# Kernel tuning notes

Measured on AMD Instinct MI355X. Metric: run time of the kernel, lower is better.

## Reference

```python
import jax, jax.numpy as jnp
import numpy as np

GROUPS = 4
BN_EPS = 1e-5


def conv2d(x, w, pad=0):
    return jax.lax.conv_general_dilated(x, w, (1, 1), [(pad, pad), (pad, pad)],
                                        dimension_numbers=('NCHW', 'OIHW', 'NCHW'))


def bn_infer(x, g, b, m, v):
    s = g * jax.lax.rsqrt(v + BN_EPS)
    return x * s[None, :, None, None] + (b - m * s)[None, :, None, None]


def refine_residual(x, w1, w3a, g, b, m, v, w3b):
    # RefineResidual(has_relu=True): 1x1 -> ConvBnRelu(3x3) -> 3x3 conv, residual, relu
    x1 = conv2d(x, w1)
    t = jax.nn.relu(bn_infer(conv2d(x1, w3a, pad=1), g, b, m, v))
    t = conv2d(t, w3b, pad=1)
    return jax.nn.relu(t + x1)


def grid_edges(H, W):
    # 4-connected pixel grid: right + down neighbors
    idx = np.arange(H * W).reshape(H, W)
    eu = np.concatenate([idx[:, :-1].ravel(), idx[:-1, :].ravel()]).astype(np.int32)
    ev = np.concatenate([idx[:, 1:].ravel(), idx[1:, :].ravel()]).astype(np.int32)
    return jnp.asarray(eu), jnp.asarray(ev)


def boruvka_mst(w, eu, ev, N):
    # Boruvka MST over the grid graph; returns bool mask over edges (N-1 True).
    E = w.shape[0]
    nodes = jnp.arange(N, dtype=jnp.int32)
    order = jnp.argsort(w).astype(jnp.int32)                  # edge ids by weight (unique ranks)
    rank = jnp.zeros(E, jnp.int32).at[order].set(jnp.arange(E, dtype=jnp.int32))
    BIG = jnp.int32(E)
    R = int(np.ceil(np.log2(max(N, 2)))) + 2

    def flatten(p):
        return jax.lax.fori_loop(0, R, lambda _, q: q[q], p)

    def body(_, state):
        parent, mst = state
        cu, cv = parent[eu], parent[ev]
        key = jnp.where(cu != cv, rank, BIG)
        cmin = jnp.minimum(jax.ops.segment_min(key, cu, num_segments=N),
                           jax.ops.segment_min(key, cv, num_segments=N))
        valid = cmin < BIG
        e = order[jnp.minimum(cmin, E - 1)]                   # min outgoing edge per component
        mst = mst.at[e].max(valid)
        other = jnp.where(cu[e] == nodes, cv[e], cu[e])
        pnew = jnp.where(valid, other, nodes)
        # break mutual (2-cycle) merges: smaller label becomes root
        pnew = jnp.where((pnew[pnew] == nodes) & (nodes < pnew), nodes, pnew)
        return flatten(pnew), mst

    _, mst = jax.lax.fori_loop(0, R + 2, body, (nodes, jnp.zeros(E, bool)))
    return mst


def root_and_depth(mst, eu, ev, N):
    # BFS-root the tree at node 0 -> parent pointers, then depth by pointer doubling.
    pn = jnp.full(N, -1, jnp.int32).at[0].set(0)

    def bfs(_, pn):
        vis = pn >= 0
        a = mst & vis[eu] & (~vis[ev])
        b = mst & vis[ev] & (~vis[eu])
        pn = pn.at[ev].max(jnp.where(a, eu, jnp.int32(-1)))
        pn = pn.at[eu].max(jnp.where(b, ev, jnp.int32(-1)))
        return pn

    pn = jax.lax.fori_loop(0, N, bfs, pn)
    R = int(np.ceil(np.log2(max(N, 2)))) + 2
    d0 = (jnp.arange(N) != 0).astype(jnp.int32)

    def dbl(_, s):
        d, p = s
        return d + d[p], p[p]

    depth, _ = jax.lax.fori_loop(0, R, dbl, (d0, pn))
    return pn, depth


def tree_filter_group(x, w, pn, depth):
    # Exact O(N) two-pass tree filter: y_i = sum_j prod(path weights i->j) x_j.
    # x: [N, C] (ones channel appended by caller), w: [N] edge weight to parent.
    N = x.shape[0]
    notroot = jnp.arange(N) != 0

    def up(i, agg):                                           # leaves -> root
        lev = N - 1 - i
        sel = (depth == lev) & notroot
        return agg.at[pn].add(jnp.where(sel[:, None], w[:, None] * agg, 0.0))

    agg = jax.lax.fori_loop(0, N - 1, up, x)

    def down(lev, F):                                         # root -> leaves
        cand = agg + w[:, None] * (F[pn] - w[:, None] * agg)
        return jnp.where(((depth == lev) & notroot)[:, None], cand, F)

    return jax.lax.fori_loop(1, N, down, agg)


def tree_filter_2d(feat, emb, pn, depth):
    # Grouped normalized tree filtering (TreeFilter2D): per-group edge affinity
    # exp(-||e_v - e_parent(v)||^2); normalize by filtering an all-ones channel.
    B, C, H, W = feat.shape
    N = H * W
    f = feat.reshape(B, GROUPS, C // GROUPS, N)
    e = emb.reshape(B, GROUPS, -1, N)

    def per_batch(fb, eb, pnb, db):
        w = jnp.exp(-jnp.sum((eb - eb[:, :, pnb]) ** 2, axis=1))   # [G, N]
        x = jnp.concatenate([fb, jnp.ones_like(fb[:, :1])], axis=1)
        x = jnp.swapaxes(x, 1, 2)                                  # [G, N, Cg+1]
        out = jax.vmap(lambda xg, wg: tree_filter_group(xg, wg, pnb, db))(x, w)
        y = out[..., :-1] / out[..., -1:]
        return jnp.swapaxes(y, 1, 2)

    out = jax.vmap(per_batch)(f, e, pn, depth)
    return out.reshape(B, C, H, W)


def _forward(fm, last_fm, lat_w1, lat_w3a, lat_g, lat_b, lat_m, lat_v, lat_w3b,
             ref_w1, ref_w3a, ref_g, ref_b, ref_m, ref_v, ref_w3b, emb_w):
    B, Cb, H, W = fm.shape
    N = H * W
    eu, ev = grid_edges(H, W)
    latent = refine_residual(fm, lat_w1, lat_w3a, lat_g, lat_b, lat_m, lat_v, lat_w3b)
    # MinimumSpanningTree(norm2_distance) on backbone features fm
    f = fm.reshape(B, Cb, N)
    dist = jnp.sum((f[:, :, eu] - f[:, :, ev]) ** 2, axis=1)       # [B, E]
    mst = jax.vmap(lambda d: boruvka_mst(d, eu, ev, N))(dist)
    pn, depth = jax.vmap(lambda m: root_and_depth(m, eu, ev, N))(mst)
    embed = conv2d(last_fm, emb_w)                                 # embed_layer (1x1, no bn/relu)
    fusion = latent + tree_filter_2d(last_fm, embed, pn, depth)
    return refine_residual(fusion, ref_w1, ref_w3a, ref_g, ref_b, ref_m, ref_v, ref_w3b)


def setup_inputs() -> dict:
    key = jax.random.key(0)
    ks = jax.random.split(key, 12)
    B, Cb, Cbiz, Cemb, H, W = 2, 1024, 64, 32, 32, 32
    r = lambda k, s: jax.random.normal(k, s, jnp.float32) * 0.05
    return dict(
        fm=jax.random.normal(ks[0], (B, Cb, H, W), jnp.float32),
        last_fm=jax.random.normal(ks[1], (B, Cbiz, H, W), jnp.float32),
        lat_w1=r(ks[2], (Cbiz, Cb, 1, 1)),
        lat_w3a=r(ks[3], (Cbiz, Cbiz, 3, 3)),
        lat_g=jnp.ones(Cbiz, jnp.float32),
        lat_b=jnp.zeros(Cbiz, jnp.float32),
        lat_m=jnp.zeros(Cbiz, jnp.float32),
        lat_v=jax.random.uniform(ks[4], (Cbiz,), jnp.float32, 0.5, 1.5),
        lat_w3b=r(ks[5], (Cbiz, Cbiz, 3, 3)),
        ref_w1=r(ks[6], (Cbiz, Cbiz, 1, 1)),
        ref_w3a=r(ks[7], (Cbiz, Cbiz, 3, 3)),
        ref_g=jnp.ones(Cbiz, jnp.float32),
        ref_b=jnp.zeros(Cbiz, jnp.float32),
        ref_m=jnp.zeros(Cbiz, jnp.float32),
        ref_v=jax.random.uniform(ks[8], (Cbiz,), jnp.float32, 0.5, 1.5),
        ref_w3b=r(ks[9], (Cbiz, Cbiz, 3, 3)),
        emb_w=r(ks[10], (Cemb, Cbiz, 1, 1)),
    )


def reference(fm, last_fm, lat_w1, lat_w3a, lat_g, lat_b, lat_m, lat_v, lat_w3b,
              ref_w1, ref_w3a, ref_g, ref_b, ref_m, ref_v, ref_w3b, emb_w):
    return _forward(fm, last_fm, lat_w1, lat_w3a, lat_g, lat_b, lat_m, lat_v, lat_w3b,
                    ref_w1, ref_w3a, ref_g, ref_b, ref_m, ref_v, ref_w3b, emb_w)
```

## Files before the change

### kernel.cpp

```cpp
#include <hip/hip_runtime.h>
#include <hip/hip_bf16.h>

#define NN 1024
#define EE 1984

__device__ __forceinline__ void edge_uv(int e, int* u, int* v) {
    if (e < 992) {
        int r = e / 31, c = e - r * 31;
        *u = r * 32 + c; *v = *u + 1;
    } else {
        *u = e - 992; *v = *u + 32;
    }
}

__device__ void conv1x1_tile(const float* __restrict__ in, const float* __restrict__ in2,
                             const float* __restrict__ w,
                             float* __restrict__ out, int CIN, int Cout,
                             int b, int co0, int n0, float* red) {
    int tid = threadIdx.x;
    int px = tid & 63, kc = tid >> 6;
    int kcu = __builtin_amdgcn_readfirstlane(kc);
    int KCH = CIN >> 4;
    size_t ibase = (size_t)b * CIN * NN + n0 + px;
    const float* wr = w + (size_t)co0 * CIN;
    float acc[8] = {0.f,0.f,0.f,0.f,0.f,0.f,0.f,0.f};
    for (int ci = kcu * KCH; ci < kcu * KCH + KCH; ++ci) {
        float xv = in[ibase + (size_t)ci * NN];
        if (in2) xv += in2[ibase + (size_t)ci * NN];
#pragma unroll
        for (int j = 0; j < 8; ++j)
            acc[j] += wr[j * CIN + ci] * xv;
    }
#pragma unroll
    for (int j = 0; j < 8; ++j) red[j * 1024 + tid] = acc[j];
    __syncthreads();
    for (int s = 8; s >= 1; s >>= 1) {
        if (kc < s) {
#pragma unroll
            for (int j = 0; j < 8; ++j)
                red[j * 1024 + kc * 64 + px] += red[j * 1024 + (kc + s) * 64 + px];
        }
        __syncthreads();
    }
    if (kc == 0) {
        size_t ob = ((size_t)b * Cout + co0) * NN + n0 + px;
#pragma unroll
        for (int j = 0; j < 8; ++j) out[ob + (size_t)j * NN] = red[j * 1024 + px];
    }
}

__device__ void dist_tile(const float* __restrict__ fm, float* __restrict__ dist,
                          int b, int eb, float* red) {
    int tid = threadIdx.x;
    int le = tid & 63, kc = tid >> 6;
    int kcu = __builtin_amdgcn_readfirstlane(kc);
    int e = eb * 64 + le;
    int u, v; edge_uv(e, &u, &v);
    const float* fp = fm + (size_t)b * 1024 * NN;
    float s = 0.f;
    for (int c = kcu * 64; c < kcu * 64 + 64; ++c) {
        float d = fp[(size_t)c * NN + u] - fp[(size_t)c * NN + v];
        s += d * d;
    }
    red[tid] = s;
    __syncthreads();
    for (int ss = 8; ss >= 1; ss >>= 1) {
        if (kc < ss) red[kc * 64 + le] += red[(kc + ss) * 64 + le];
        __syncthreads();
    }
    if (kc == 0) dist[b * EE + e] = red[le];
}

__device__ void conv3x3_body(const float* __restrict__ in, const float* __restrict__ w,
                             const float* __restrict__ gg, const float* __restrict__ bb,
                             const float* __restrict__ mm, const float* __restrict__ vv,
                             const float* __restrict__ res, float* __restrict__ out,
                             int mode, int b, int co, int r0, float* pl) {
    int tid = threadIdx.x;
    const float* ip = in + (size_t)b * 64 * NN;
    const float* wp = w + (size_t)co * 64 * 9;
    int r = tid >> 5, c = tid & 31;
    float acc = 0.f;
    for (int h = 0; h < 2; ++h) {
        __syncthreads();
        for (int i4 = tid; i4 < 32 * 80; i4 += 256) {
            int ci = i4 / 80, o = i4 - ci * 80;
            int row = r0 - 1 + (o >> 3), c4 = (o & 7) << 2;
            float4 val = make_float4(0.f, 0.f, 0.f, 0.f);
            if (row >= 0 && row < 32)
                val = *(const float4*)&ip[(size_t)(h * 32 + ci) * NN + row * 32 + c4];
            *(float4*)&pl[ci * 320 + (o >> 3) * 32 + c4] = val;
        }
        __syncthreads();
        for (int ci = 0; ci < 32; ++ci) {
            float wv[9];
#pragma unroll
            for (int q = 0; q < 9; ++q) wv[q] = wp[(h * 32 + ci) * 9 + q];
            float s = 0.f;
#pragma unroll
            for (int dy = 0; dy < 3; ++dy) {
                const float* row = &pl[ci * 320 + (r + dy) * 32];
#pragma unroll
                for (int dx = -1; dx <= 1; ++dx) {
                    int cc = c + dx;
                    float xv = (cc >= 0 && cc < 32) ? row[cc] : 0.f;
                    s += wv[dy * 3 + (dx + 1)] * xv;
                }
            }
            acc += s;
        }
    }
    float val;
    size_t op = ((size_t)b * 64 + co) * NN + r0 * 32 + tid;
    if (mode == 0) {
        float sc = gg[co] * rsqrtf(vv[co] + 1e-5f);
        val = acc * sc + (bb[co] - mm[co] * sc);
    } else {
        val = acc + res[op];
    }
    out[op] = fmaxf(val, 0.f);
}

struct MstS {
    unsigned long long minkey[NN];
    unsigned long long ekey[EE];
    int parent[NN], pnw[NN], pn[NN], dep[NN], scr[NN], elist[NN];
    int mstm[EE];
    int cnt, cnt2;
};

__device__ void mst_body_1024(const float* __restrict__ dist, int b, MstS* S,
                              int* __restrict__ pn_g, int* __restrict__ maxd_g,
                              int* __restrict__ ord_g, int* __restrict__ off_g) {
    int tid = threadIdx.x;
    const float* wb = dist + b * EE;
    S->parent[tid] = tid;
    S->minkey[tid] = ~0ULL;
    for (int e = tid; e < EE; e += 1024) {
        S->mstm[e] = 0;
        S->ekey[e] = ((unsigned long long)__float_as_uint(wb[e]) << 32) | (unsigned)e;
    }
    if (tid == 0) { S->cnt = 0; S->cnt2 = 0; }
    __syncthreads();

    int r = tid >> 5, c = tid & 31;
    int* P = S->parent;
    int* Q = S->pnw;
    for (int round = 0; round < 14; ++round) {
        int pv = P[tid];
        unsigned long long mk = ~0ULL;
        if (c < 31 && P[tid + 1] != pv) {
            unsigned long long k = S->ekey[r * 31 + c]; if (k < mk) mk = k;
        }
        if (c > 0 && P[tid - 1] != pv) {
            unsigned long long k = S->ekey[r * 31 + c - 1]; if (k < mk) mk = k;
        }
        if (r < 31 && P[tid + 32] != pv) {
            unsigned long long k = S->ekey[992 + r * 32 + c]; if (k < mk) mk = k;
        }
        if (r > 0 && P[tid - 32] != pv) {
            unsigned long long k = S->ekey[992 + (r - 1) * 32 + c]; if (k < mk) mk = k;
        }
        if (mk != ~0ULL) atomicMin(&S->minkey[pv], mk);
        __syncthreads();

        unsigned long long sel = S->minkey[tid];
        int np;
        if (sel != ~0ULL) {
            int e = (int)(sel & 0xffffffffULL);
            if (atomicExch(&S->mstm[e], 1) == 0) atomicAdd(&S->cnt, 1);
            int eu, ev; edge_uv(e, &eu, &ev);
            int cu = P[eu], cv = P[ev];
            np = (cu == tid) ? cv : cu;
        } else np = tid;
        int q = np, pq;
        if (q == tid) pq = tid;
        else {
            unsigned long long selq = S->minkey[q];
            if (selq != ~0ULL) {
                int e2 = (int)(selq & 0xffffffffULL);
                int eu2, ev2; edge_uv(e2, &eu2, &ev2);
                int cu2 = P[eu2], cv2 = P[ev2];
                pq = (cu2 == q) ? cv2 : cu2;
            } else pq = q;
        }
        Q[tid] = (pq == tid && tid < q) ? tid : q;
        __syncthreads();

        bool first = true;
        for (;;) {
            if (first) { S->minkey[tid] = ~0ULL; first = false; }
            int p = Q[tid];
            p = Q[p]; p = Q[p]; p = Q[p];
            Q[tid] = p;
            int ch = (Q[p] != p);
            if (!__syncthreads_or(ch)) break;
        }
        if (S->cnt == NN - 1) break;
        int* t = P; P = Q; Q = t;
    }

    for (int e = tid; e < EE; e += 1024)
        if (S->mstm[e]) { int s = atomicAdd(&S->cnt2, 1); S->elist[s] = e; }
    __syncthreads();
    int ecnt = S->cnt2;

    S->pn[tid] = (tid == 0) ? 0 : -1;
    __syncthreads();
    volatile int* vpn = S->pn;
    int myu = 0, myv = 0; bool have = tid < ecnt;
    if (have) { edge_uv(S->elist[tid], &myu, &myv); }
    for (;;) {
        int ch = 0;
        for (int s = 0; s < 24; ++s) {
            if (have) {
                int pu = vpn[myu], pv = vpn[myv];
                if (pu >= 0 && pv < 0)      { vpn[myv] = myu; ch = 1; }
                else if (pv >= 0 && pu < 0) { vpn[myu] = myv; ch = 1; }
            }
        }
        if (!__syncthreads_or(ch)) break;
    }
    int incomplete = __syncthreads_or(S->pn[tid] < 0);

    S->dep[tid] = (tid != 0) ? 1 : 0;
    S->pnw[tid] = S->pn[tid];
    __syncthreads();
    int* dA = S->dep;  int* dB = (int*)S->ekey;
    int* pA = S->pnw;  int* pB = ((int*)S->ekey) + NN;
    for (int it = 0; it < 12; ++it) {
        int p = pA[tid];
        int j = (p < 0) ? (NN + p) : p;
        dB[tid] = dA[tid] + dA[j];
        int nx = pA[j];
        pB[tid] = nx;
        int anynz = __syncthreads_or(nx != 0);
        int* t = dA; dA = dB; dB = t;
        t = pA; pA = pB; pB = t;
        if (!incomplete && !anynz) break;
    }
    if (tid == 0) S->cnt = 0;
    __syncthreads();
    int d = dA[tid];
    if (d >= 1 && d <= NN - 1) atomicMax(&S->cnt, d);
    __syncthreads();
    int maxd = S->cnt;

    S->scr[tid] = 0;
    __syncthreads();
    int bkt = (tid != 0 && d >= 1 && d <= NN - 1) ? d : 0;
    atomicAdd(&S->scr[bkt], 1);
    __syncthreads();
    int cntv = S->scr[tid];
    int lane = tid & 63, wid = tid >> 6;
    int x = cntv;
    for (int d2 = 1; d2 < 64; d2 <<= 1) {
        int y = __shfl_up(x, d2, 64);
        if (lane >= d2) x += y;
    }
    if (lane == 63) S->pnw[wid] = x;
    __syncthreads();
    if (tid < 16) {
        int off = 0;
        for (int i = 0; i < tid; ++i) off += S->pnw[i];
        S->parent[tid] = off;
    }
    __syncthreads();
    int excl = x - cntv + S->parent[wid];
    int* mi = (int*)S->minkey;
    mi[tid] = excl;
    S->scr[tid] = excl;
    __syncthreads();
    int pos = atomicAdd(&S->scr[bkt], 1);
    S->elist[pos] = tid;
    __syncthreads();

    pn_g[b * NN + tid]    = S->pn[tid];
    ord_g[b * NN + tid]   = S->elist[tid];
    off_g[b * 1025 + tid] = mi[tid];
    if (tid == 0) { off_g[b * 1025 + 1024] = NN; maxd_g[b] = maxd; }
}

struct TfSmem { float agg[NN * 3]; float wv[NN]; int jj[NN]; int ords[NN]; int offs[1025]; };
__device__ void treefilter_wave(const float* __restrict__ feat, const float* __restrict__ emb,
                                const int* __restrict__ pn_g, const int* __restrict__ ord_g,
                                const int* __restrict__ off_g, const int* __restrict__ maxd_g,
                                float* __restrict__ tfout, int b, int g, int sub, TfSmem* S) {
    int lane = threadIdx.x;
    const float* eb = emb + ((size_t)b * 32 + g * 8) * NN;
    int c0 = g * 16 + sub * 2;
    const float* fb = feat + ((size_t)b * 64 + c0) * NN;
    for (int k = 0; k < 16; ++k) {
        int v = lane + k * 64;
        int p = pn_g[b * NN + v];
        int j = (p < 0) ? (NN + p) : p;
        S->jj[v] = j;
        float s = 0.f;
#pragma unroll
        for (int q = 0; q < 8; ++q) {
            float d = eb[(size_t)q * NN + v] - eb[(size_t)q * NN + j];
            s += d * d;
        }
        S->wv[v] = expf(-s);
        S->agg[v * 3 + 0] = fb[v];
        S->agg[v * 3 + 1] = fb[NN + v];
        S->agg[v * 3 + 2] = 1.f;
        S->ords[v] = ord_g[b * NN + v];
        S->offs[v] = off_g[b * 1025 + v];
    }
    if (lane == 0) S->offs[1024] = NN;
    int maxdep = maxd_g[b];
    for (int lev = maxdep; lev >= 1; --lev) {
        int s0 = S->offs[lev], s1 = S->offs[lev + 1];
        for (int i = s0 + lane; i < s1; i += 64) {
            int v = S->ords[i]; int j = S->jj[v]; float w = S->wv[v];
            atomicAdd(&S->agg[j * 3 + 0], w * S->agg[v * 3 + 0]);
            atomicAdd(&S->agg[j * 3 + 1], w * S->agg[v * 3 + 1]);
            atomicAdd(&S->agg[j * 3 + 2], w * S->agg[v * 3 + 2]);
        }
    }
    for (int lev = 1; lev <= maxdep; ++lev) {
        int s0 = S->offs[lev], s1 = S->offs[lev + 1];
        for (int i = s0 + lane; i < s1; i += 64) {
            int v = S->ords[i]; int j = S->jj[v]; float w = S->wv[v];
#pragma unroll
            for (int c = 0; c < 3; ++c) {
                float a = S->agg[v * 3 + c];
                S->agg[v * 3 + c] = a + w * (S->agg[j * 3 + c] - w * a);
            }
        }
    }
    float* ob = tfout + ((size_t)b * 64 + c0) * NN;
    for (int k = 0; k < 16; ++k) {
        int v = lane + k * 64;
        float inv = 1.f / S->agg[v * 3 + 2];
        ob[v]      = S->agg[v * 3 + 0] * inv;
        ob[NN + v] = S->agg[v * 3 + 1] * inv;
    }
}

__global__ __launch_bounds__(1024) void k0_dist(
    const float* __restrict__ fm, float* __restrict__ dist) {
    __shared__ float red[1024];
    int i = blockIdx.x;
    dist_tile(fm, dist, i / 31, i % 31, red);
}

union K1S { float red[8192]; MstS m; };
__global__ __launch_bounds__(1024) void k1_fused(
    const float* __restrict__ fm, const float* __restrict__ last_fm,
    const float* __restrict__ lat_w1, const float* __restrict__ emb_w,
    float* __restrict__ lat_x1, float* __restrict__ embed,
    const float* __restrict__ dist, int* __restrict__ pn_g,
    int* __restrict__ maxd_g, int* __restrict__ ord_g, int* __restrict__ off_g) {
    __shared__ __align__(16) K1S s;
    int bx = blockIdx.x;
    if (bx < 2) {
        mst_body_1024(dist, bx, &s.m, pn_g, maxd_g, ord_g, off_g);
    } else if (bx < 258) {
        int i = bx - 2, b = i >> 7, r = i & 127;
        conv1x1_tile(fm, nullptr, lat_w1, lat_x1, 1024, 64,
                     b, (r >> 4) * 8, (r & 15) * 64, s.red);
    } else {
        int i = bx - 258, b = i >> 6, r = i & 63;
        conv1x1_tile(last_fm, nullptr, emb_w, embed, 64, 32,
                     b, (r >> 4) * 8, (r & 15) * 64, s.red);
    }
}

union K2S { float pl[32 * 320]; TfSmem t; };
__global__ __launch_bounds__(256) void k2_fused(
    const float* __restrict__ lat_x1, const float* __restrict__ lat_w3a,
    const float* __restrict__ lat_g, const float* __restrict__ lat_b,
    const float* __restrict__ lat_m, const float* __restrict__ lat_v,
    float* __restrict__ lat_t1,
    const float* __restrict__ last_fm, const float* __restrict__ embed,
    const int* __restrict__ pn_g, const int* __restrict__ ord_g,
    const int* __restrict__ off_g, const int* __restrict__ maxd_g,
    float* __restrict__ tfout) {
    __shared__ __align__(16) K2S s;
    int bx = blockIdx.x;
    if (bx < 64) {
        if (threadIdx.x >= 64) return;
        treefilter_wave(last_fm, embed, pn_g, ord_g, off_g, maxd_g, tfout,
                        bx >> 5, (bx >> 3) & 3, bx & 7, &s.t);
    } else {
        int i = bx - 64, b = i >> 8, co = (i >> 2) & 63, r0 = (i & 3) * 8;
        conv3x3_body(lat_x1, lat_w3a, lat_g, lat_b, lat_m, lat_v,
                     nullptr, lat_t1, 0, b, co, r0, s.pl);
    }
}

__global__ __launch_bounds__(256) void conv3x3_kernel(
    const float* __restrict__ in, const float* __restrict__ w,
    const float* __restrict__ gg, const float* __restrict__ bb,
    const float* __restrict__ mm, const float* __restrict__ vv,
    const float* __restrict__ res, float* __restrict__ out, int mode) {
    __shared__ __align__(16) float pl[32 * 320];
    conv3x3_body(in, w, gg, bb, mm, vv, res, out, mode,
                 blockIdx.z, blockIdx.y, blockIdx.x * 8, pl);
}

__global__ __launch_bounds__(1024) void conv1x1_add_kernel(
    const float* __restrict__ in, const float* __restrict__ in2,
    const float* __restrict__ w, float* __restrict__ out, int CIN, int Cout) {
    __shared__ float red[8192];
    conv1x1_tile(in, in2, w, out, CIN, Cout, blockIdx.z, blockIdx.y * 8,
                 blockIdx.x * 64, red);
}

extern "C" void kernel_launch(void* const* d_in, const int* in_sizes, int n_in,
                              void* d_out, int out_size, void* d_ws, size_t ws_size,
                              hipStream_t stream) {
    const float* fm      = (const float*)d_in[0];
    const float* last_fm = (const float*)d_in[1];
    const float* lat_w1  = (const float*)d_in[2];
    const float* lat_w3a = (const float*)d_in[3];
    const float* lat_g   = (const float*)d_in[4];
    const float* lat_b   = (const float*)d_in[5];
    const float* lat_m   = (const float*)d_in[6];
    const float* lat_v   = (const float*)d_in[7];
    const float* lat_w3b = (const float*)d_in[8];
    const float* ref_w1  = (const float*)d_in[9];
    const float* ref_w3a = (const float*)d_in[10];
    const float* ref_g   = (const float*)d_in[11];
    const float* ref_b   = (const float*)d_in[12];
    const float* ref_m   = (const float*)d_in[13];
    const float* ref_v   = (const float*)d_in[14];
    const float* ref_w3b = (const float*)d_in[15];
    const float* emb_w   = (const float*)d_in[16];
    float* out = (float*)d_out;

    float* ws      = (float*)d_ws;
    float* lat_x1  = ws;
    float* lat_t1  = lat_x1 + 131072;
    float* latent  = lat_t1 + 131072;
    float* dist    = latent + 131072;
    float* embed   = dist + 4096;
    float* tfout   = embed + 65536;
    float* ref_x1  = tfout + 131072;
    float* ref_t1  = ref_x1 + 131072;
    int*   pn      = (int*)(ref_t1 + 131072);
    int*   ordg    = pn + 2048;
    int*   offg    = ordg + 2048;
    int*   maxd    = offg + 2080;

    k0_dist<<<62, 1024, 0, stream>>>(fm, dist);
    k1_fused<<<386, 1024, 0, stream>>>(fm, last_fm, lat_w1, emb_w,
                                       lat_x1, embed, dist, pn, maxd, ordg, offg);
    k2_fused<<<576, 256, 0, stream>>>(lat_x1, lat_w3a, lat_g, lat_b, lat_m, lat_v,
                                      lat_t1, last_fm, embed, pn, ordg, offg,
                                      maxd, tfout);
    conv3x3_kernel<<<dim3(4, 64, 2), 256, 0, stream>>>(
        lat_t1, lat_w3b, nullptr, nullptr, nullptr, nullptr, lat_x1, latent, 1);
    conv1x1_add_kernel<<<dim3(16, 8, 2), 1024, 0, stream>>>(
        latent, tfout, ref_w1, ref_x1, 64, 64);
    conv3x3_kernel<<<dim3(4, 64, 2), 256, 0, stream>>>(
        ref_x1, ref_w3a, ref_g, ref_b, ref_m, ref_v, nullptr, ref_t1, 0);
    conv3x3_kernel<<<dim3(4, 64, 2), 256, 0, stream>>>(
        ref_t1, ref_w3b, nullptr, nullptr, nullptr, nullptr, ref_x1, out, 1);
}
```

Before: 244.3 us.

## Fold refine 1x1 into 3x3 weights and regroup stages into five launches

Precomputes a contracted weight (ref_w3a composed with ref_w1) so the refine 3x3 conv reads latent+tfout directly instead of waiting on the 1x1 output. That 3x3 conv then runs alongside the 1x1 in one launch. The stages are regrouped so that dist and lat 1x1 share the first kernel, the MST overlaps the lat 3x3a conv (now full-image 1024-thread blocks), and the lat 3x3b conv overlaps the tree filter. The goal is fewer launches and more overlap of the serial MST and tree-filter work with convs. The cost is extra FLOPs for the contraction and added 3x3 work on 64 input channels.

Measured after the change: 226.5 us. 7.3% less time.

```diff
diff --git a/kernel.cpp b/kernel.cpp
--- a/kernel.cpp
+++ b/kernel.cpp
@@ -13,7 +13,7 @@
     }
 }
 
-__device__ void conv1x1_tile(const float* __restrict__ in, const float* __restrict__ in2,
+__device__ void conv1x1_tile(const float* __restrict__ in,
                              const float* __restrict__ w,
                              float* __restrict__ out, int CIN, int Cout,
                              int b, int co0, int n0, float* red) {
@@ -26,7 +26,6 @@
     float acc[8] = {0.f,0.f,0.f,0.f,0.f,0.f,0.f,0.f};
     for (int ci = kcu * KCH; ci < kcu * KCH + KCH; ++ci) {
         float xv = in[ibase + (size_t)ci * NN];
-        if (in2) xv += in2[ibase + (size_t)ci * NN];
 #pragma unroll
         for (int j = 0; j < 8; ++j)
             acc[j] += wr[j * CIN + ci] * xv;
@@ -47,6 +46,24 @@
 #pragma unroll
         for (int j = 0; j < 8; ++j) out[ob + (size_t)j * NN] = red[j * 1024 + px];
     }
+}
+
+__device__ void conv1x1_64(const float* __restrict__ in, const float* __restrict__ in2,
+                           const float* __restrict__ w, float* __restrict__ out,
+                           int b, int co0, int px0) {
+    int tid = threadIdx.x;
+    size_t ibase = (size_t)b * 64 * NN + px0 + tid;
+    const float* wr = w + (size_t)co0 * 64;
+    float acc[8] = {0.f,0.f,0.f,0.f,0.f,0.f,0.f,0.f};
+    for (int ci = 0; ci < 64; ++ci) {
+        float xv = in[ibase + (size_t)ci * NN] + in2[ibase + (size_t)ci * NN];
+#pragma unroll
+        for (int j = 0; j < 8; ++j)
+            acc[j] += wr[j * 64 + ci] * xv;
+    }
+    size_t ob = ((size_t)b * 64 + co0) * NN + px0 + tid;
+#pragma unroll
+    for (int j = 0; j < 8; ++j) out[ob + (size_t)j * NN] = acc[j];
 }
 
 __device__ void dist_tile(const float* __restrict__ fm, float* __restrict__ dist,
@@ -71,13 +88,26 @@
     if (kc == 0) dist[b * EE + e] = red[le];
 }
 
-__device__ void conv3x3_body(const float* __restrict__ in, const float* __restrict__ w,
+__device__ void wc_contract(const float* __restrict__ w3a, const float* __restrict__ w1,
+                            float* __restrict__ wc, int co) {
+    int t = threadIdx.x;
+    if (t >= 576) return;
+    int ci = t / 9, q = t - ci * 9;
+    float s = 0.f;
+    for (int cm = 0; cm < 64; ++cm)
+        s += w3a[((size_t)co * 64 + cm) * 9 + q] * w1[cm * 64 + ci];
+    wc[((size_t)co * 64 + ci) * 9 + q] = s;
+}
+
+__device__ void conv3x3_body(const float* __restrict__ in, const float* __restrict__ in2,
+                             const float* __restrict__ w,
                              const float* __restrict__ gg, const float* __restrict__ bb,
                              const float* __restrict__ mm, const float* __restrict__ vv,
                              const float* __restrict__ res, float* __restrict__ out,
                              int mode, int b, int co, int r0, float* pl) {
     int tid = threadIdx.x;
     const float* ip = in + (size_t)b * 64 * NN;
+    const float* ip2 = in2 ? in2 + (size_t)b * 64 * NN : nullptr;
     const float* wp = w + (size_t)co * 64 * 9;
     int r = tid >> 5, c = tid & 31;
     float acc = 0.f;
@@ -87,8 +117,14 @@
             int ci = i4 / 80, o = i4 - ci * 80;
             int row = r0 - 1 + (o >> 3), c4 = (o & 7) << 2;
             float4 val = make_float4(0.f, 0.f, 0.f, 0.f);
-            if (row >= 0 && row < 32)
-                val = *(const float4*)&ip[(size_t)(h * 32 + ci) * NN + row * 32 + c4];
+            if (row >= 0 && row < 32) {
+                size_t off = (size_t)(h * 32 + ci) * NN + row * 32 + c4;
+                val = *(const float4*)&ip[off];
+                if (ip2) {
+                    float4 v2 = *(const float4*)&ip2[off];
+                    val.x += v2.x; val.y += v2.y; val.z += v2.z; val.w += v2.w;
+                }
+            }
             *(float4*)&pl[ci * 320 + (o >> 3) * 32 + c4] = val;
         }
         __syncthreads();
@@ -112,6 +148,55 @@
     }
     float val;
     size_t op = ((size_t)b * 64 + co) * NN + r0 * 32 + tid;
+    if (mode == 0) {
+        float sc = gg[co] * rsqrtf(vv[co] + 1e-5f);
+        val = acc * sc + (bb[co] - mm[co] * sc);
+    } else {
+        val = acc + res[op];
+    }
+    out[op] = fmaxf(val, 0.f);
+}
+
+__device__ void conv3x3_1024(const float* __restrict__ in, const float* __restrict__ w,
+                             const float* __restrict__ gg, const float* __restrict__ bb,
+                             const float* __restrict__ mm, const float* __restrict__ vv,
+                             const float* __restrict__ res, float* __restrict__ out,
+                             int mode, int b, int co, float* pl) {
+    int tid = threadIdx.x;
+    int r = tid >> 5, c = tid & 31;
+    const float* ip = in + (size_t)b * 64 * NN;
+    const float* wp = w + (size_t)co * 64 * 9;
+    float acc = 0.f;
+    for (int h = 0; h < 8; ++h) {
+        __syncthreads();
+        for (int i4 = tid; i4 < 2048; i4 += 1024) {
+            int ci = i4 >> 8, o4 = (i4 & 255) << 2;
+            *(float4*)&pl[ci * 1024 + o4] =
+                *(const float4*)&ip[(size_t)(h * 8 + ci) * NN + o4];
+        }
+        __syncthreads();
+        for (int ci = 0; ci < 8; ++ci) {
+            float wv[9];
+#pragma unroll
+            for (int q = 0; q < 9; ++q) wv[q] = wp[(h * 8 + ci) * 9 + q];
+            const float* P = &pl[ci * 1024];
+            float s = 0.f;
+#pragma unroll
+            for (int dy = -1; dy <= 1; ++dy) {
+                int rr = r + dy;
+                if (rr < 0 || rr >= 32) continue;
+#pragma unroll
+                for (int dx = -1; dx <= 1; ++dx) {
+                    int cc = c + dx;
+                    float xv = (cc >= 0 && cc < 32) ? P[rr * 32 + cc] : 0.f;
+                    s += wv[(dy + 1) * 3 + (dx + 1)] * xv;
+                }
+            }
+            acc += s;
+        }
+    }
+    float val;
+    size_t op = ((size_t)b * 64 + co) * NN + tid;
     if (mode == 0) {
         float sc = gg[co] * rsqrtf(vv[co] + 1e-5f);
         val = acc * sc + (bb[co] - mm[co] * sc);
@@ -339,45 +424,56 @@
     }
 }
 
-__global__ __launch_bounds__(1024) void k0_dist(
-    const float* __restrict__ fm, float* __restrict__ dist) {
-    __shared__ float red[1024];
-    int i = blockIdx.x;
-    dist_tile(fm, dist, i / 31, i % 31, red);
-}
-
-union K1S { float red[8192]; MstS m; };
+__global__ __launch_bounds__(1024) void k0_fused(
+    const float* __restrict__ fm, const float* __restrict__ lat_w1,
+    const float* __restrict__ ref_w3a, const float* __restrict__ ref_w1,
+    float* __restrict__ lat_x1, float* __restrict__ dist, float* __restrict__ wc) {
+    __shared__ __align__(16) float red[8192];
+    int bx = blockIdx.x;
+    if (bx < 62) {
+        dist_tile(fm, dist, bx / 31, bx % 31, red);
+    } else if (bx < 318) {
+        int i = bx - 62, b = i >> 7, r = i & 127;
+        conv1x1_tile(fm, lat_w1, lat_x1, 1024, 64,
+                     b, (r >> 4) * 8, (r & 15) * 64, red);
+    } else {
+        wc_contract(ref_w3a, ref_w1, wc, bx - 318);
+    }
+}
+
+union K1S { float red[8192]; float pl[8192]; MstS m; };
 __global__ __launch_bounds__(1024) void k1_fused(
-    const float* __restrict__ fm, const float* __restrict__ last_fm,
-    const float* __restrict__ lat_w1, const float* __restrict__ emb_w,
-    float* __restrict__ lat_x1, float* __restrict__ embed,
     const float* __restrict__ dist, int* __restrict__ pn_g,
-    int* __restrict__ maxd_g, int* __restrict__ ord_g, int* __restrict__ off_g) {
+    int* __restrict__ maxd_g, int* __restrict__ ord_g, int* __restrict__ off_g,
+    const float* __restrict__ lat_x1, const float* __restrict__ lat_w3a,
+    const float* __restrict__ lat_g, const float* __restrict__ lat_b,
+    const float* __restrict__ lat_m, const float* __restrict__ lat_v,
+    float* __restrict__ lat_t1,
+    const float* __restrict__ last_fm, const float* __restrict__ emb_w,
+    float* __restrict__ embed) {
     __shared__ __align__(16) K1S s;
     int bx = blockIdx.x;
     if (bx < 2) {
         mst_body_1024(dist, bx, &s.m, pn_g, maxd_g, ord_g, off_g);
-    } else if (bx < 258) {
-        int i = bx - 2, b = i >> 7, r = i & 127;
-        conv1x1_tile(fm, nullptr, lat_w1, lat_x1, 1024, 64,
-                     b, (r >> 4) * 8, (r & 15) * 64, s.red);
-    } else {
-        int i = bx - 258, b = i >> 6, r = i & 63;
-        conv1x1_tile(last_fm, nullptr, emb_w, embed, 64, 32,
+    } else if (bx < 130) {
+        int t = bx - 2;
+        conv3x3_1024(lat_x1, lat_w3a, lat_g, lat_b, lat_m, lat_v,
+                     nullptr, lat_t1, 0, t >> 6, t & 63, s.pl);
+    } else {
+        int i = bx - 130, b = i >> 6, r = i & 63;
+        conv1x1_tile(last_fm, emb_w, embed, 64, 32,
                      b, (r >> 4) * 8, (r & 15) * 64, s.red);
     }
 }
 
 union K2S { float pl[32 * 320]; TfSmem t; };
 __global__ __launch_bounds__(256) void k2_fused(
-    const float* __restrict__ lat_x1, const float* __restrict__ lat_w3a,
-    const float* __restrict__ lat_g, const float* __restrict__ lat_b,
-    const float* __restrict__ lat_m, const float* __restrict__ lat_v,
-    float* __restrict__ lat_t1,
     const float* __restrict__ last_fm, const float* __restrict__ embed,
     const int* __restrict__ pn_g, const int* __restrict__ ord_g,
     const int* __restrict__ off_g, const int* __restrict__ maxd_g,
-    float* __restrict__ tfout) {
+    float* __restrict__ tfout,
+    const float* __restrict__ lat_t1, const float* __restrict__ lat_w3b,
+    const float* __restrict__ lat_x1, float* __restrict__ latent) {
     __shared__ __align__(16) K2S s;
     int bx = blockIdx.x;
     if (bx < 64) {
@@ -386,27 +482,38 @@
                         bx >> 5, (bx >> 3) & 3, bx & 7, &s.t);
     } else {
         int i = bx - 64, b = i >> 8, co = (i >> 2) & 63, r0 = (i & 3) * 8;
-        conv3x3_body(lat_x1, lat_w3a, lat_g, lat_b, lat_m, lat_v,
-                     nullptr, lat_t1, 0, b, co, r0, s.pl);
-    }
-}
-
-__global__ __launch_bounds__(256) void conv3x3_kernel(
-    const float* __restrict__ in, const float* __restrict__ w,
-    const float* __restrict__ gg, const float* __restrict__ bb,
-    const float* __restrict__ mm, const float* __restrict__ vv,
-    const float* __restrict__ res, float* __restrict__ out, int mode) {
+        conv3x3_body(lat_t1, nullptr, lat_w3b, nullptr, nullptr, nullptr, nullptr,
+                     lat_x1, latent, 1, b, co, r0, s.pl);
+    }
+}
+
+__global__ __launch_bounds__(256) void k3_fused(
+    const float* __restrict__ latent, const float* __restrict__ tfout,
+    const float* __restrict__ wc,
+    const float* __restrict__ ref_g, const float* __restrict__ ref_b,
+    const float* __restrict__ ref_m, const float* __restrict__ ref_v,
+    const float* __restrict__ ref_w1,
+    float* __restrict__ ref_t1, float* __restrict__ ref_x1) {
     __shared__ __align__(16) float pl[32 * 320];
-    conv3x3_body(in, w, gg, bb, mm, vv, res, out, mode,
-                 blockIdx.z, blockIdx.y, blockIdx.x * 8, pl);
-}
-
-__global__ __launch_bounds__(1024) void conv1x1_add_kernel(
-    const float* __restrict__ in, const float* __restrict__ in2,
-    const float* __restrict__ w, float* __restrict__ out, int CIN, int Cout) {
-    __shared__ float red[8192];
-    conv1x1_tile(in, in2, w, out, CIN, Cout, blockIdx.z, blockIdx.y * 8,
-                 blockIdx.x * 64, red);
+    int bx = blockIdx.x;
+    if (bx < 512) {
+        int b = bx >> 8, co = (bx >> 2) & 63, r0 = (bx & 3) * 8;
+        conv3x3_body(latent, tfout, wc, ref_g, ref_b, ref_m, ref_v,
+                     nullptr, ref_t1, 0, b, co, r0, pl);
+    } else {
+        int i = bx - 512, b = i >> 5, co0 = ((i >> 2) & 7) * 8, px0 = (i & 3) * 256;
+        conv1x1_64(latent, tfout, ref_w1, ref_x1, b, co0, px0);
+    }
+}
+
+__global__ __launch_bounds__(256) void k4_tail(
+    const float* __restrict__ ref_t1, const float* __restrict__ ref_w3b,
+    const float* __restrict__ ref_x1, float* __restrict__ out) {
+    __shared__ __align__(16) float pl[32 * 320];
+    int bx = blockIdx.x;
+    int b = bx >> 8, co = (bx >> 2) & 63, r0 = (bx & 3) * 8;
+    conv3x3_body(ref_t1, nullptr, ref_w3b, nullptr, nullptr, nullptr, nullptr,
+                 ref_x1, out, 1, b, co, r0, pl);
 }
 
 extern "C" void kernel_launch(void* const* d_in, const int* in_sizes, int n_in,
@@ -440,23 +547,21 @@
     float* tfout   = embed + 65536;
     float* ref_x1  = tfout + 131072;
     float* ref_t1  = ref_x1 + 131072;
-    int*   pn      = (int*)(ref_t1 + 131072);
+    float* wc      = ref_t1 + 131072;
+    int*   pn      = (int*)(wc + 36992);
     int*   ordg    = pn + 2048;
     int*   offg    = ordg + 2048;
     int*   maxd    = offg + 2080;
 
-    k0_dist<<<62, 1024, 0, stream>>>(fm, dist);
-    k1_fused<<<386, 1024, 0, stream>>>(fm, last_fm, lat_w1, emb_w,
-                                       lat_x1, embed, dist, pn, maxd, ordg, offg);
-    k2_fused<<<576, 256, 0, stream>>>(lat_x1, lat_w3a, lat_g, lat_b, lat_m, lat_v,
-                                      lat_t1, last_fm, embed, pn, ordg, offg,
-                                      maxd, tfout);
-    conv3x3_kernel<<<dim3(4, 64, 2), 256, 0, stream>>>(
-        lat_t1, lat_w3b, nullptr, nullptr, nullptr, nullptr, lat_x1, latent, 1);
-    conv1x1_add_kernel<<<dim3(16, 8, 2), 1024, 0, stream>>>(
-        latent, tfout, ref_w1, ref_x1, 64, 64);
-    conv3x3_kernel<<<dim3(4, 64, 2), 256, 0, stream>>>(
-        ref_x1, ref_w3a, ref_g, ref_b, ref_m, ref_v, nullptr, ref_t1, 0);
-    conv3x3_kernel<<<dim3(4, 64, 2), 256, 0, stream>>>(
-        ref_t1, ref_w3b, nullptr, nullptr, nullptr, nullptr, ref_x1, out, 1);
-}
+    k0_fused<<<382, 1024, 0, stream>>>(fm, lat_w1, ref_w3a, ref_w1,
+                                       lat_x1, dist, wc);
+    k1_fused<<<258, 1024, 0, stream>>>(dist, pn, maxd, ordg, offg,
+                                       lat_x1, lat_w3a, lat_g, lat_b, lat_m, lat_v,
+                                       lat_t1, last_fm, emb_w, embed);
+    k2_fused<<<576, 256, 0, stream>>>(last_fm, embed, pn, ordg, offg, maxd,
+                                      tfout, lat_t1, lat_w3b, lat_x1, latent);
+    k3_fused<<<576, 256, 0, stream>>>(latent, tfout, wc,
+                                      ref_g, ref_b, ref_m, ref_v, ref_w1,
+                                      ref_t1, ref_x1);
+    k4_tail<<<512, 256, 0, stream>>>(ref_t1, ref_w3b, ref_x1, out);
+}
```
